# Optimization experiments

Measured on AMD Instinct MI355X. Metric: run time of the kernel, lower is better.

## Reference

```python
import jax, jax.numpy as jnp
import numpy as np

N_HASHES = 4
CHUNK = 144
REDUCTION = 4

# PyTorch bicubic (a=-0.75), align_corners=False, integer scale 2 ->
# fixed fractional offsets t=0.75 (even outputs) and t=0.25 (odd outputs).
_EW = jnp.array([-0.03515625, 0.26171875, 0.87890625, -0.10546875], jnp.float32)
_OW = _EW[::-1]


def _up2_axis(x, axis):
    n = x.shape[axis]
    pad = [(0, 0)] * x.ndim
    pad[axis] = (2, 2)
    xp = jnp.pad(x, pad, mode='edge')  # torch clamps border indices
    sl = lambda s: jax.lax.slice_in_dim(xp, s, s + n, axis=axis)
    even = sum(_EW[k] * sl(k) for k in range(4))
    odd = sum(_OW[k] * sl(k + 1) for k in range(4))
    out = jnp.stack([even, odd], axis=axis + 1)
    shp = list(x.shape)
    shp[axis] = 2 * n
    return out.reshape(shp)


def bicubic_up2(x):
    return _up2_axis(_up2_axis(x, 2), 3)


def conv2d(x, w, b, pad):
    y = jax.lax.conv_general_dilated(x, w, (1, 1), [(pad, pad), (pad, pad)],
                                     dimension_numbers=('NCHW', 'OIHW', 'NCHW'))
    return y + b[None, :, None, None]


def _adj(t):
    # attend to own + two adjacent buckets along chunk axis (axis=2)
    return jnp.concatenate([t, jnp.roll(t, 1, axis=2), jnp.roll(t, -1, axis=2)], axis=3)


def nlsa(x, wm, bm, wa, ba, rot):
    N, Cc, H, W = x.shape
    L = H * W
    xe = conv2d(x, wm, bm, 1).reshape(N, -1, L).transpose(0, 2, 1)  # [N,L,C]
    ye = conv2d(x, wa, ba, 0).reshape(N, -1, L).transpose(0, 2, 1)  # [N,L,C*red]
    C = xe.shape[-1]
    hash_buckets = min(L // CHUNK + (L // CHUNK) % 2, 128)
    # LSH: random rotations -> argmax bucket codes (non-differentiable, detached)
    rotated = jnp.einsum('btf,fhi->bhti', xe, rot)  # [N,h,L,hb//2]
    rotated = jnp.concatenate([rotated, -rotated], axis=-1)  # [N,h,L,hb]
    codes = jnp.argmax(rotated, axis=-1)  # [N,h,L]
    codes = codes + (jnp.arange(N_HASHES) * hash_buckets)[None, :, None]
    codes = jax.lax.stop_gradient(codes.reshape(N, -1))  # [N,h*L]
    indices = jnp.argsort(codes, axis=-1)
    undo = jnp.argsort(indices, axis=-1)
    mod = indices % L
    xs = jnp.take_along_axis(xe, mod[..., None], axis=1)  # [N,h*L,C]
    ys = jnp.take_along_axis(ye, mod[..., None], axis=1)  # [N,h*L,C*red]
    padding = (-L) % CHUNK
    xb = xs.reshape(N, N_HASHES, L, C)
    yb = ys.reshape(N, N_HASHES, L, C * REDUCTION)
    if padding:
        xb = jnp.concatenate([xb, xb[:, :, -padding:, :]], axis=2)
        yb = jnp.concatenate([yb, yb[:, :, -padding:, :]], axis=2)
    nch = xb.shape[2] // CHUNK
    xb = xb.reshape(N, N_HASHES, nch, CHUNK, C)
    yb = yb.reshape(N, N_HASHES, nch, CHUNK, C * REDUCTION)
    xm = xb / jnp.maximum(jnp.linalg.norm(xb, axis=-1, keepdims=True), 5e-5)
    xm = _adj(xm)      # [N,h,k,3*chunk,C]
    ybj = _adj(yb)     # [N,h,k,3*chunk,C*red]
    raw = jnp.einsum('bhkie,bhkje->bhkij', xb, xm)  # [N,h,k,chunk,3*chunk]
    bscore = jax.scipy.special.logsumexp(raw, axis=-1, keepdims=True)
    score = jnp.exp(raw - bscore)
    ret = jnp.einsum('bhkij,bhkje->bhkie', score, ybj)
    ret = ret.reshape(N, N_HASHES, -1, C * REDUCTION)
    bscore = bscore.reshape(N, N_HASHES, -1)
    if padding:
        ret = ret[:, :, :-padding]
        bscore = bscore[:, :, :-padding]
    ret = ret.reshape(N, -1, C * REDUCTION)
    bscore = bscore.reshape(N, -1)
    ret = jnp.take_along_axis(ret, undo[..., None], axis=1)
    bscore = jnp.take_along_axis(bscore, undo, axis=1)
    ret = ret.reshape(N, N_HASHES, L, C * REDUCTION)
    probs = jax.nn.softmax(bscore.reshape(N, N_HASHES, L, 1), axis=1)
    ret = jnp.sum(ret * probs, axis=1)  # [N,L,C*red]
    return ret.transpose(0, 2, 1).reshape(N, -1, H, W) + x


def setup_inputs() -> dict:
    key = jax.random.key(0)
    ks = jax.random.split(key, 8)
    w = lambda k, shape, fan: (jax.random.normal(k, shape, jnp.float32) / np.sqrt(fan)).astype(jnp.float32)
    return {
        'x': jax.random.normal(ks[0], (2, 64, 96, 96), jnp.float32),
        'w1': w(ks[1], (64, 64, 3, 3), 64 * 9), 'b1': jnp.zeros((64,), jnp.float32),
        'w2': w(ks[2], (64, 64, 3, 3), 64 * 9), 'b2': jnp.zeros((64,), jnp.float32),
        'wm': w(ks[3], (16, 64, 3, 3), 64 * 9), 'bm': jnp.zeros((16,), jnp.float32),
        'wa': w(ks[4], (64, 64, 1, 1), 64), 'ba': jnp.zeros((64,), jnp.float32),
        'rot': jax.random.normal(ks[5], (16, N_HASHES, 64), jnp.float32),  # [C, h, hash_buckets//2]
    }


def reference(x, w1, b1, w2, b2, wm, bm, wa, ba, rot):
    x = bicubic_up2(x)
    x = jax.nn.relu(conv2d(x, w1, b1, 1))
    x = jax.nn.relu(conv2d(x, w2, b2, 1))
    return nlsa(x, wm, bm, wa, ba, rot)
```

## Files before the change

kernel.cpp:

```cpp
#include <hip/hip_runtime.h>
#include <math.h>

#define NB 2
#define CIN 64
#define H0 96
#define W0 96
#define HH 192
#define WW 192
#define LL (HH*WW)
#define NHASH 4
#define CHK 144
#define NCHK 256
#define CE 16
#define CV 64
#define NBUCK 128
#define SEGL 576
#define NSEG 64

#define K_ROWB   80
#define V_ROWB   912
#define P_ROWB   72
#define KQ_SZB   34560
#define VT_SZB   58368
#define PST_SZB  10368
#define LKI_SZB  1728
#define QN_SZB   576
#define LDS_T2   (KQ_SZB + VT_SZB + PST_SZB + LKI_SZB + QN_SZB)
#define LDS_T1   (VT_SZB + LKI_SZB)

typedef __attribute__((ext_vector_type(8))) short short8_t;
typedef __attribute__((ext_vector_type(4))) float f32x4;
union FragU { unsigned int u[4]; int4 i; short8_t s; };

__device__ __forceinline__ unsigned int cvtpk_bf16(float a, float b){
  unsigned int r;
  asm("v_cvt_pk_bf16_f32 %0, %1, %2" : "=v"(r) : "v"(a), "v"(b));
  return r;
}
__device__ __forceinline__ float bfl(unsigned int u){ return __uint_as_float(u << 16); }
__device__ __forceinline__ float bfh(unsigned int u){ return __uint_as_float(u & 0xffff0000u); }

__global__ __launch_bounds__(256) void k_upsample(const float* __restrict__ x,
                                                  float* __restrict__ out){
  int idx = blockIdx.x*256 + threadIdx.x;
  if (idx >= NB*CIN*HH*WW) return;
  int ox = idx % WW; int t2 = idx / WW;
  int oy = t2 % HH;  t2 /= HH;
  int i = oy >> 1, a = oy & 1;
  int j = ox >> 1, b = ox & 1;
  const float e0=-0.03515625f, e1=0.26171875f, e2=0.87890625f, e3=-0.10546875f;
  float wy[4], wx[4]; int ty[4], tx[4];
  if (a){ wy[0]=e3; wy[1]=e2; wy[2]=e1; wy[3]=e0; } else { wy[0]=e0; wy[1]=e1; wy[2]=e2; wy[3]=e3; }
  if (b){ wx[0]=e3; wx[1]=e2; wx[2]=e1; wx[3]=e0; } else { wx[0]=e0; wx[1]=e1; wx[2]=e2; wx[3]=e3; }
  int offy = a ? -1 : -2, offx = b ? -1 : -2;
  #pragma unroll
  for (int k=0;k<4;k++){
    int t = i + offy + k; ty[k] = t<0?0:(t>H0-1?H0-1:t);
    int s = j + offx + k; tx[k] = s<0?0:(s>W0-1?W0-1:s);
  }
  const float* xp = x + (size_t)t2*H0*W0;
  float s = 0.f;
  #pragma unroll
  for (int ky=0;ky<4;ky++){
    const float* row = xp + ty[ky]*W0;
    float rs = 0.f;
    rs = fmaf(wx[0], row[tx[0]], rs);
    rs = fmaf(wx[1], row[tx[1]], rs);
    rs = fmaf(wx[2], row[tx[2]], rs);
    rs = fmaf(wx[3], row[tx[3]], rs);
    s = fmaf(wy[ky], rs, s);
  }
  out[idx] = s;
}

__global__ __launch_bounds__(256) void k_prepw(const float* __restrict__ w,
    unsigned short* __restrict__ wsT, int CO){
  int idx = blockIdx.x*256 + threadIdx.x;
  if (idx >= CO*64*9) return;
  int tap = idx % 9; int rem = idx / 9;
  int ci = rem % 64; int co = rem / 64;
  float v = w[(size_t)(co*64 + ci)*9 + tap];
  unsigned int hu = cvtpk_bf16(v, v) & 0xffffu;
  float hf = bfl(hu);
  unsigned int lu = cvtpk_bf16(v - hf, 0.f) & 0xffffu;
  int half = ci >> 5, kg = (ci >> 3) & 3, e = ci & 7;
  size_t base = ((size_t)(tap*2 + half)*2)*CO*32 + ((size_t)co*4 + kg)*8 + e;
  wsT[base]         = (unsigned short)hu;
  wsT[base + (size_t)CO*32] = (unsigned short)lu;
}

template<int CO, bool RELU, bool OUT_NLC>
__global__ __launch_bounds__(256) void k_conv3m(const float* __restrict__ in,
    const unsigned short* __restrict__ wsT, const float* __restrict__ bias,
    float* __restrict__ out){
  __shared__ unsigned short inH[3][66][64];
  __shared__ unsigned short inL[3][66][64];
  const int t = threadIdx.x;
  const int bx = blockIdx.x, y = blockIdx.y, n = blockIdx.z;
  const int x0 = bx*64;
  const int l = t & 63, w = t >> 6;
  const int lq = l & 15, kg = l >> 4;

  for (int e = t; e < 3072; e += 256){
    const int chunk = e & 15;
    const int strip = e >> 4;
    const int ci = strip & 63, row = strip >> 6;
    const int gy = y + row - 1;
    float4 v = make_float4(0.f,0.f,0.f,0.f);
    if (gy >= 0 && gy < HH)
      v = *(const float4*)&in[(((size_t)n*CIN + ci)*HH + gy)*WW + x0 + chunk*4];
    float vv[4] = {v.x, v.y, v.z, v.w};
    #pragma unroll
    for (int j = 0; j < 4; ++j){
      const int col = 1 + chunk*4 + j;
      const int sci = (((ci >> 3) ^ (col & 7)) << 3) | (ci & 7);
      unsigned int hu = cvtpk_bf16(vv[j], vv[j]);
      unsigned int lu = cvtpk_bf16(vv[j] - bfl(hu), 0.f);
      inH[row][col][sci] = (unsigned short)hu;
      inL[row][col][sci] = (unsigned short)lu;
    }
  }
  if (t < 192){
    const int ci = t & 63, row = t >> 6;
    const int gy = y + row - 1;
    const bool okY = (gy >= 0 && gy < HH);
    const float* ip = &in[(((size_t)n*CIN + ci)*HH + (size_t)(okY?gy:0))*WW];
    float vL = (okY && x0 >= 1) ? ip[x0-1] : 0.f;
    float vR = (okY && x0+64 < WW) ? ip[x0+64] : 0.f;
    unsigned int hL = cvtpk_bf16(vL, vL);
    unsigned int lLu = cvtpk_bf16(vL - bfl(hL), 0.f);
    unsigned int hR = cvtpk_bf16(vR, vR);
    unsigned int lRu = cvtpk_bf16(vR - bfl(hR), 0.f);
    const int sci0 = ci;
    const int sci65 = (((ci >> 3) ^ 1) << 3) | (ci & 7);
    inH[row][0][sci0]  = (unsigned short)hL;  inL[row][0][sci0]  = (unsigned short)lLu;
    inH[row][65][sci65] = (unsigned short)hR; inL[row][65][sci65] = (unsigned short)lRu;
  }
  __syncthreads();

  constexpr int NCT = CO/16;
  f32x4 acc[NCT];
  #pragma unroll
  for (int c=0;c<NCT;c++) acc[c] = (f32x4){0.f,0.f,0.f,0.f};
  const unsigned short* wlane = wsT + (size_t)lq*32 + (size_t)kg*8;

  #pragma unroll
  for (int tap=0; tap<9; ++tap){
    const int ky = tap/3, kx = tap - ky*3;
    const int col = w*16 + lq + kx;
    #pragma unroll
    for (int half=0; half<2; ++half){
      const int sci = ((((half<<2) | kg) ^ (col & 7)) << 3);
      FragU Bh, Bl;
      Bh.i = *(const int4*)&inH[ky][col][sci];
      Bl.i = *(const int4*)&inL[ky][col][sci];
      const unsigned short* wth = wlane + (size_t)((tap*2+half)*2)*CO*32;
      #pragma unroll
      for (int ct=0; ct<NCT; ++ct){
        FragU Ah, Al;
        Ah.i = *(const int4*)(wth + ct*512);
        Al.i = *(const int4*)(wth + CO*32 + ct*512);
        acc[ct] = __builtin_amdgcn_mfma_f32_16x16x32_bf16(Ah.s, Bl.s, acc[ct], 0,0,0);
        acc[ct] = __builtin_amdgcn_mfma_f32_16x16x32_bf16(Al.s, Bh.s, acc[ct], 0,0,0);
        acc[ct] = __builtin_amdgcn_mfma_f32_16x16x32_bf16(Ah.s, Bh.s, acc[ct], 0,0,0);
      }
    }
  }

  const int px = x0 + w*16 + lq;
  if constexpr (!OUT_NLC){
    #pragma unroll
    for (int ct=0; ct<NCT; ++ct){
      #pragma unroll
      for (int r=0; r<4; ++r){
        const int co = ct*16 + kg*4 + r;
        float v = acc[ct][r] + bias[co];
        if (RELU) v = fmaxf(v, 0.f);
        out[(((size_t)n*CO + co)*HH + y)*WW + px] = v;
      }
    }
  } else {
    #pragma unroll
    for (int r=0; r<4; ++r){
      const int co = kg*4 + r;
      float v = acc[0][r] + bias[co];
      if (RELU) v = fmaxf(v, 0.f);
      out[((size_t)n*LL + y*WW + px)*CO + co] = v;
    }
  }
}

__global__ __launch_bounds__(256) void k_conv1x1(const float* __restrict__ x2,
    const float* __restrict__ wa, const float* __restrict__ ba,
    unsigned short* __restrict__ yeB){
  __shared__ float xs[64][64];
  __shared__ float wts[64][64];
  const int t = threadIdx.x;
  const int n = blockIdx.y;
  const int l0 = blockIdx.x*64;
  for (int e=t; e<4096; e+=256){
    int ci = e >> 6, l = e & 63;
    xs[ci][l]  = x2[((size_t)n*CIN+ci)*LL + l0 + l];
    wts[ci][l] = wa[(size_t)l*64 + ci];
  }
  __syncthreads();
  const int l = t & 63, cq = t >> 6;
  float acc[16];
  #pragma unroll
  for (int i=0;i<16;i++) acc[i] = ba[cq*16+i];
  for (int ci=0; ci<64; ci++){
    float xv = xs[ci][l];
    #pragma unroll
    for (int i=0;i<16;i++) acc[i] = fmaf(xv, wts[ci][cq*16+i], acc[i]);
  }
  unsigned int wds[8];
  #pragma unroll
  for (int i=0;i<8;i++) wds[i] = cvtpk_bf16(acc[2*i], acc[2*i+1]);
  uint4* op = (uint4*)&yeB[((size_t)n*LL + l0 + l)*64 + cq*16];
  op[0] = make_uint4(wds[0],wds[1],wds[2],wds[3]);
  op[1] = make_uint4(wds[4],wds[5],wds[6],wds[7]);
}

__global__ __launch_bounds__(128) void k_codes(const float* __restrict__ xe,
    const float* __restrict__ rot, unsigned char* __restrict__ codes){
  __shared__ float rs[NHASH][64][16];
  const int t = threadIdx.x;
  for (int e=t; e<4096; e+=128){
    int f = e >> 8; int rem = e & 255;
    int h = rem >> 6; int i = rem & 63;
    rs[h][i][f] = rot[((size_t)f*NHASH + h)*64 + i];
  }
  __syncthreads();
  const int n = blockIdx.y;
  const int l = blockIdx.x*128 + t;
  float q[16];
  const float* xr = &xe[((size_t)n*LL + l)*16];
  #pragma unroll
  for (int f=0;f<16;f++) q[f] = xr[f];
  #pragma unroll
  for (int h=0;h<NHASH;h++){
    float bp = -3.0e38f, bn = -3.0e38f; int ap=0, an=0;
    for (int i=0;i<64;i++){
      float s = 0.f;
      #pragma unroll
      for (int f=0;f<16;f++) s = fmaf(q[f], rs[h][i][f], s);
      if (s > bp){ bp = s; ap = i; }
      if (-s > bn){ bn = -s; an = i; }
    }
    int code = (bp >= bn) ? ap : (64 + an);
    codes[((size_t)n*NHASH + h)*LL + l] = (unsigned char)code;
  }
}

__global__ __launch_bounds__(256) void k_hist(const unsigned char* __restrict__ codes,
    unsigned int* __restrict__ segHist){
  __shared__ unsigned int h[NBUCK];
  const int t = threadIdx.x;
  if (t < NBUCK) h[t] = 0;
  __syncthreads();
  const int n = blockIdx.z, hh = blockIdx.y, s = blockIdx.x;
  const unsigned char* cp = codes + ((size_t)n*NHASH + hh)*LL + (size_t)s*SEGL;
  for (int e=t; e<SEGL; e+=256) atomicAdd(&h[cp[e]], 1u);
  __syncthreads();
  if (t < NBUCK)
    segHist[(((size_t)(n*NHASH+hh))*NSEG + s)*NBUCK + t] = h[t];
}

__global__ __launch_bounds__(128) void k_scan(unsigned int* __restrict__ segHist){
  __shared__ unsigned int tot[NBUCK];
  __shared__ unsigned int base[NBUCK];
  const int b = threadIdx.x;
  const size_t off = (size_t)blockIdx.x * NSEG * NBUCK;
  unsigned int run = 0;
  for (int s=0;s<NSEG;s++){
    unsigned int v = segHist[off + (size_t)s*NBUCK + b];
    segHist[off + (size_t)s*NBUCK + b] = run;
    run += v;
  }
  tot[b] = run;
  __syncthreads();
  if (b==0){ unsigned int r=0; for (int i=0;i<NBUCK;i++){ base[i]=r; r+=tot[i]; } }
  __syncthreads();
  const unsigned int bb = base[b];
  for (int s=0;s<NSEG;s++) segHist[off + (size_t)s*NBUCK + b] += bb;
}

__global__ __launch_bounds__(256) void k_rank(const unsigned char* __restrict__ codes,
    const unsigned int* __restrict__ segHist, int* __restrict__ srtIdx){
  __shared__ unsigned int cw[SEGL/4];
  __shared__ unsigned int sbase[NBUCK];
  const int t = threadIdx.x;
  const int n = blockIdx.z, hh = blockIdx.y, s = blockIdx.x;
  const size_t cb = ((size_t)n*NHASH + hh)*LL + (size_t)s*SEGL;
  const unsigned int* cp32 = (const unsigned int*)(codes + cb);
  for (int e=t; e<SEGL/4; e+=256) cw[e] = cp32[e];
  if (t < NBUCK)
    sbase[t] = segHist[(((size_t)(n*NHASH+hh))*NSEG + s)*NBUCK + t];
  __syncthreads();
  const size_t ob = ((size_t)n*NHASH + hh)*LL;
  for (int e=t; e<SEGL; e+=256){
    unsigned int c = (cw[e>>2] >> ((e&3)*8)) & 0xffu;
    unsigned int mul = c * 0x01010101u;
    int cnt = 0;
    const int nw = e >> 2;
    for (int wi=0; wi<nw; wi++){
      unsigned int v = cw[wi] ^ mul;
      unsigned int t1 = (v & 0x7f7f7f7fu) + 0x7f7f7f7fu;
      unsigned int z = ~(t1 | v) & 0x80808080u;
      cnt += __popc(z);
    }
    unsigned int lastw = cw[nw];
    const int nbp = e & 3;
    for (int bp=0; bp<nbp; bp++)
      if (((lastw >> (bp*8)) & 0xffu) == c) cnt++;
    int pos = (int)sbase[c] + cnt;
    srtIdx[ob + pos] = s*SEGL + e;
  }
}

__global__ __launch_bounds__(256) void k_gatherK(const float* __restrict__ xe,
    const int* __restrict__ srtIdx, unsigned short* __restrict__ Ksrt,
    float* __restrict__ normQ){
  const int idx = blockIdx.x*256 + threadIdx.x;
  if (idx >= NB*NHASH*LL) return;
  const int n = idx / (NHASH*LL);
  const int lk = srtIdx[idx];
  const float4* xr = (const float4*)&xe[((size_t)n*LL + lk)*16];
  float4 v0 = xr[0], v1 = xr[1], v2 = xr[2], v3 = xr[3];
  float f[16] = {v0.x,v0.y,v0.z,v0.w, v1.x,v1.y,v1.z,v1.w,
                 v2.x,v2.y,v2.z,v2.w, v3.x,v3.y,v3.z,v3.w};
  float ss = 0.f;
  #pragma unroll
  for (int i=0;i<16;i++) ss = fmaf(f[i], f[i], ss);
  const float nq = sqrtf(ss);
  normQ[idx] = nq;
  const float inv = 1.f / fmaxf(nq, 5e-5f);
  #pragma unroll
  for (int i=0;i<16;i++) f[i] *= inv;
  unsigned int kh[8], klo[8];
  #pragma unroll
  for (int i=0;i<8;i++) kh[i] = cvtpk_bf16(f[2*i], f[2*i+1]);
  #pragma unroll
  for (int i=0;i<8;i++)
    klo[i] = cvtpk_bf16(f[2*i] - bfl(kh[i]), f[2*i+1] - bfh(kh[i]));
  int4* kr = (int4*)(Ksrt + (size_t)idx*32);
  kr[0] = make_int4((int)kh[0],(int)kh[1],(int)kh[2],(int)kh[3]);
  kr[1] = make_int4((int)kh[4],(int)kh[5],(int)kh[6],(int)kh[7]);
  kr[2] = make_int4((int)klo[0],(int)klo[1],(int)klo[2],(int)klo[3]);
  kr[3] = make_int4((int)klo[4],(int)klo[5],(int)klo[6],(int)klo[7]);
}

__global__ __launch_bounds__(576) void k_attn2t1(const unsigned short* __restrict__ yeB,
    const int* __restrict__ srtIdx, const unsigned short* __restrict__ Ksrt,
    const float* __restrict__ normQ, unsigned short* __restrict__ retS,
    float* __restrict__ bscore){
  extern __shared__ char smem[];
  char* Vt  = smem;
  int* lkI  = (int*)(smem + VT_SZB);
  __shared__ char PstA[9][1024];
  __shared__ char PstB[9][1024];

  const int t = threadIdx.x;
  const int k = blockIdx.x, hh = blockIdx.y, n = blockIdx.z;
  const size_t sb = ((size_t)n*NHASH + hh)*LL;
  const int l = t & 63, w = t >> 6;
  const int lq16 = l & 15, g = l >> 4;

  if (t < 432){
    const int c3 = t / CHK, jl = t - c3*CHK;
    const int kc = (c3==0) ? k : ((c3==1) ? ((k+NCHK-1)&(NCHK-1)) : ((k+1)&(NCHK-1)));
    lkI[t] = srtIdx[sb + (size_t)kc*CHK + jl];
  }
  if (t < 512){
    int c = t >> 3, jp = t & 7;
    *(unsigned int*)(Vt + c*V_ROWB + 864 + jp*4) = 0u;
  }
  __syncthreads();

  #pragma unroll 4
  for (int it=0; it<24; ++it){
    const int e = t + it*576;
    const int jp = e >> 6, c = e & 63;
    const unsigned int a = yeB[((size_t)n*LL + lkI[2*jp  ])*64 + c];
    const unsigned int b = yeB[((size_t)n*LL + lkI[2*jp+1])*64 + c];
    *(unsigned int*)(Vt + c*V_ROWB + jp*4) = a | (b << 16);
  }
  const int qg = w*16 + lq16;
  const int pq = k*CHK + qg;
  const int lqs = lkI[qg];
  FragU b1, b2;
  const unsigned short* qrow = Ksrt + (sb + pq)*32;
  b1.i = *(const int4*)(qrow + (g&1)*8);
  if (g < 2) b2.i = *(const int4*)(qrow + 16 + (g&1)*8);
  else { b2.u[0]=0u; b2.u[1]=0u; b2.u[2]=0u; b2.u[3]=0u; }
  const float nq_ = normQ[sb + pq];
  const float msc = fmaxf(nq_, 5e-5f);
  __syncthreads();

  float sum = 0.f;
  char* const pwA = &PstA[w][0];
  char* const pwB = &PstB[w][0];
  const int pws = lq16*64 + (g&1)*8;
  const int prd = lq16*64 + ((g ^ (lq16&3))<<4);

  auto qksub = [&](int u, char* __restrict__ pw){
    #pragma unroll
    for (int sub=0; sub<2; ++sub){
      const int t27 = 2*u + sub;
      uint2 pwv;
      if (t27 < 27){
        const int c3 = t27 / 9;
        const int kc = (c3==0) ? k : ((c3==1) ? ((k+NCHK-1)&(NCHK-1)) : ((k+1)&(NCHK-1)));
        const int row16 = (t27 - c3*9)*16;
        FragU a; a.i = *(const int4*)(Ksrt + (sb + (size_t)kc*CHK + row16 + lq16)*32 + g*8);
        f32x4 C = {0.f,0.f,0.f,0.f};
        C = __builtin_amdgcn_mfma_f32_16x16x32_bf16(a.s, b2.s, C, 0, 0, 0);
        C = __builtin_amdgcn_mfma_f32_16x16x32_bf16(a.s, b1.s, C, 0, 0, 0);
        const float p0 = __expf(fmaf(msc, C[0], -nq_));
        const float p1 = __expf(fmaf(msc, C[1], -nq_));
        const float p2 = __expf(fmaf(msc, C[2], -nq_));
        const float p3 = __expf(fmaf(msc, C[3], -nq_));
        sum += (p0+p1) + (p2+p3);
        pwv = make_uint2(cvtpk_bf16(p0,p1), cvtpk_bf16(p2,p3));
      } else {
        pwv = make_uint2(0u, 0u);
      }
      const int chunk = (sub*2 + (g>>1)) ^ (lq16 & 3);
      *(uint2*)(pw + pws + (chunk<<4)) = pwv;
    }
  };

  f32x4 O0 = {0.f,0.f,0.f,0.f}, O1 = O0, O2 = O0, O3 = O0;
  qksub(0, pwA);
  #pragma unroll
  for (int uu=0; uu<7; ++uu){
    {
      const int u = 2*uu;
      const char* Vb = Vt + lq16*V_ROWB + u*64 + g*16;
      FragU av0, av1, av2, av3;
      av0.i = *(const int4*)(Vb);
      av1.i = *(const int4*)(Vb + 16*V_ROWB);
      av2.i = *(const int4*)(Vb + 32*V_ROWB);
      av3.i = *(const int4*)(Vb + 48*V_ROWB);
      qksub(u+1, pwB);
      FragU bp; bp.i = *(const int4*)(pwA + prd);
      O0 = __builtin_amdgcn_mfma_f32_16x16x32_bf16(av0.s, bp.s, O0, 0,0,0);
      O1 = __builtin_amdgcn_mfma_f32_16x16x32_bf16(av1.s, bp.s, O1, 0,0,0);
      O2 = __builtin_amdgcn_mfma_f32_16x16x32_bf16(av2.s, bp.s, O2, 0,0,0);
      O3 = __builtin_amdgcn_mfma_f32_16x16x32_bf16(av3.s, bp.s, O3, 0,0,0);
    }
    {
      const int u = 2*uu + 1;
      const char* Vb = Vt + lq16*V_ROWB + u*64 + g*16;
      FragU av0, av1, av2, av3;
      av0.i = *(const int4*)(Vb);
      av1.i = *(const int4*)(Vb + 16*V_ROWB);
      av2.i = *(const int4*)(Vb + 32*V_ROWB);
      av3.i = *(const int4*)(Vb + 48*V_ROWB);
      qksub(u+1, pwA);
      FragU bp; bp.i = *(const int4*)(pwB + prd);
      O0 = __builtin_amdgcn_mfma_f32_16x16x32_bf16(av0.s, bp.s, O0, 0,0,0);
      O1 = __builtin_amdgcn_mfma_f32_16x16x32_bf16(av1.s, bp.s, O1, 0,0,0);
      O2 = __builtin_amdgcn_mfma_f32_16x16x32_bf16(av2.s, bp.s, O2, 0,0,0);
      O3 = __builtin_amdgcn_mfma_f32_16x16x32_bf16(av3.s, bp.s, O3, 0,0,0);
    }
  }
  sum += __shfl_xor(sum, 16);
  sum += __shfl_xor(sum, 32);
  const float linv = 1.f / sum;

  unsigned short* op = &retS[(sb + lqs)*64];
  {
    uint2 s0 = make_uint2(cvtpk_bf16(O0[0]*linv, O0[1]*linv), cvtpk_bf16(O0[2]*linv, O0[3]*linv));
    uint2 s1 = make_uint2(cvtpk_bf16(O1[0]*linv, O1[1]*linv), cvtpk_bf16(O1[2]*linv, O1[3]*linv));
    uint2 s2 = make_uint2(cvtpk_bf16(O2[0]*linv, O2[1]*linv), cvtpk_bf16(O2[2]*linv, O2[3]*linv));
    uint2 s3 = make_uint2(cvtpk_bf16(O3[0]*linv, O3[1]*linv), cvtpk_bf16(O3[2]*linv, O3[3]*linv));
    *(uint2*)(op +  0 + g*4) = s0;
    *(uint2*)(op + 16 + g*4) = s1;
    *(uint2*)(op + 32 + g*4) = s2;
    *(uint2*)(op + 48 + g*4) = s3;
  }
  if (g == 0) bscore[sb + lqs] = nq_ + logf(sum);
}

__global__ __launch_bounds__(576) void k_attn2b(const float* __restrict__ xe,
    const unsigned short* __restrict__ yeB, const int* __restrict__ srtIdx,
    unsigned short* __restrict__ retS, float* __restrict__ bscore){
  extern __shared__ char smem[];
  unsigned short* Kq = (unsigned short*)smem;
  char* Vt  = smem + KQ_SZB;
  char* Pst = Vt + VT_SZB;
  int* lkI  = (int*)(Pst + PST_SZB);
  float* qn = (float*)(Pst + PST_SZB + LKI_SZB);

  const int t = threadIdx.x;
  const int k = blockIdx.x, hh = blockIdx.y, n = blockIdx.z;
  const size_t sb = ((size_t)n*NHASH + hh)*LL;
  const int l = t & 63, w = t >> 6;
  const int lq16 = l & 15, g = l >> 4;

  if (t < 432){
    const int c3 = t / CHK, jl = t - c3*CHK;
    const int kc = (c3==0) ? k : ((c3==1) ? ((k+NCHK-1)&(NCHK-1)) : ((k+1)&(NCHK-1)));
    const int lk = srtIdx[sb + (size_t)kc*CHK + jl];
    lkI[t] = lk;
    const float4* xr = (const float4*)&xe[((size_t)n*LL + lk)*16];
    float4 v0 = xr[0], v1 = xr[1], v2 = xr[2], v3 = xr[3];
    float f[16] = {v0.x,v0.y,v0.z,v0.w, v1.x,v1.y,v1.z,v1.w,
                   v2.x,v2.y,v2.z,v2.w, v3.x,v3.y,v3.z,v3.w};
    float ss = 0.f;
    #pragma unroll
    for (int i=0;i<16;i++) ss = fmaf(f[i], f[i], ss);
    const float nq = sqrtf(ss);
    if (c3 == 0) qn[jl] = nq;
    const float inv = 1.f / fmaxf(nq, 5e-5f);
    #pragma unroll
    for (int i=0;i<16;i++) f[i] *= inv;
    unsigned int kh[8], klo[8];
    #pragma unroll
    for (int i=0;i<8;i++) kh[i] = cvtpk_bf16(f[2*i], f[2*i+1]);
    #pragma unroll
    for (int i=0;i<8;i++)
      klo[i] = cvtpk_bf16(f[2*i] - bfl(kh[i]), f[2*i+1] - bfh(kh[i]));
    int4* kr = (int4*)((char*)Kq + t*K_ROWB);
    kr[0] = make_int4((int)kh[0],(int)kh[1],(int)kh[2],(int)kh[3]);
    kr[1] = make_int4((int)kh[4],(int)kh[5],(int)kh[6],(int)kh[7]);
    kr[2] = make_int4((int)klo[0],(int)klo[1],(int)klo[2],(int)klo[3]);
    kr[3] = make_int4((int)klo[4],(int)klo[5],(int)klo[6],(int)klo[7]);
  }
  if (t < 512){
    int c = t >> 3, jp = t & 7;
    *(unsigned int*)(Vt + c*V_ROWB + 864 + jp*4) = 0u;
  }
  __syncthreads();

  #pragma unroll 4
  for (int it=0; it<24; ++it){
    const int e = t + it*576;
    const int jp = e >> 6, c = e & 63;
    const unsigned int a = yeB[((size_t)n*LL + lkI[2*jp  ])*64 + c];
    const unsigned int b = yeB[((size_t)n*LL + lkI[2*jp+1])*64 + c];
    *(unsigned int*)(Vt + c*V_ROWB + jp*4) = a | (b << 16);
  }
  const int qg = w*16 + lq16;
  const int lqs = lkI[qg];
  FragU b1, b2;
  float nq_;
  {
    const char* qrow = (const char*)Kq + qg*K_ROWB;
    b1.i = *(const int4*)(qrow + (g&1)*16);
    if (g < 2) b2.i = *(const int4*)(qrow + 32 + (g&1)*16);
    else { b2.u[0]=0u; b2.u[1]=0u; b2.u[2]=0u; b2.u[3]=0u; }
    nq_ = qn[qg];
  }
  const float msc = fmaxf(nq_, 5e-5f);
  __syncthreads();

  float sum = 0.f;
  f32x4 O0 = {0.f,0.f,0.f,0.f}, O1 = O0, O2 = O0, O3 = O0;
  char* Pw = Pst + w*(16*P_ROWB);
  for (int u=0; u<14; ++u){
    #pragma unroll
    for (int sub=0; sub<2; ++sub){
      const int t27 = u*2 + sub;
      uint2 pw;
      if (t27 < 27){
        FragU a;
        a.i = *(const int4*)((const char*)Kq + (size_t)(t27*16 + lq16)*K_ROWB + g*16);
        f32x4 C = {0.f,0.f,0.f,0.f};
        C = __builtin_amdgcn_mfma_f32_16x16x32_bf16(a.s, b2.s, C, 0, 0, 0);
        C = __builtin_amdgcn_mfma_f32_16x16x32_bf16(a.s, b1.s, C, 0, 0, 0);
        const float p0 = __expf(fmaf(msc, C[0], -nq_));
        const float p1 = __expf(fmaf(msc, C[1], -nq_));
        const float p2 = __expf(fmaf(msc, C[2], -nq_));
        const float p3 = __expf(fmaf(msc, C[3], -nq_));
        sum += (p0+p1) + (p2+p3);
        pw = make_uint2(cvtpk_bf16(p0,p1), cvtpk_bf16(p2,p3));
      } else {
        pw = make_uint2(0u, 0u);
      }
      *(uint2*)(Pw + lq16*P_ROWB + sub*32 + g*8) = pw;
    }
    asm volatile("s_waitcnt lgkmcnt(0)" ::: "memory");
    __builtin_amdgcn_sched_barrier(0);
    FragU bp; bp.i = *(const int4*)(Pw + lq16*P_ROWB + g*16);
    const char* Vb = Vt + lq16*V_ROWB + u*64 + g*16;
    FragU av;
    av.i = *(const int4*)(Vb);             O0 = __builtin_amdgcn_mfma_f32_16x16x32_bf16(av.s, bp.s, O0, 0,0,0);
    av.i = *(const int4*)(Vb + 16*V_ROWB); O1 = __builtin_amdgcn_mfma_f32_16x16x32_bf16(av.s, bp.s, O1, 0,0,0);
    av.i = *(const int4*)(Vb + 32*V_ROWB); O2 = __builtin_amdgcn_mfma_f32_16x16x32_bf16(av.s, bp.s, O2, 0,0,0);
    av.i = *(const int4*)(Vb + 48*V_ROWB); O3 = __builtin_amdgcn_mfma_f32_16x16x32_bf16(av.s, bp.s, O3, 0,0,0);
  }
  sum += __shfl_xor(sum, 16);
  sum += __shfl_xor(sum, 32);
  const float linv = 1.f / sum;

  unsigned short* op = &retS[(sb + lqs)*64];
  {
    uint2 s0 = make_uint2(cvtpk_bf16(O0[0]*linv, O0[1]*linv), cvtpk_bf16(O0[2]*linv, O0[3]*linv));
    uint2 s1 = make_uint2(cvtpk_bf16(O1[0]*linv, O1[1]*linv), cvtpk_bf16(O1[2]*linv, O1[3]*linv));
    uint2 s2 = make_uint2(cvtpk_bf16(O2[0]*linv, O2[1]*linv), cvtpk_bf16(O2[2]*linv, O2[3]*linv));
    uint2 s3 = make_uint2(cvtpk_bf16(O3[0]*linv, O3[1]*linv), cvtpk_bf16(O3[2]*linv, O3[3]*linv));
    *(uint2*)(op +  0 + g*4) = s0;
    *(uint2*)(op + 16 + g*4) = s1;
    *(uint2*)(op + 32 + g*4) = s2;
    *(uint2*)(op + 48 + g*4) = s3;
  }
  if (g == 0) bscore[sb + lqs] = nq_ + logf(sum);
}

__global__ __launch_bounds__(256) void k_combine(const unsigned short* __restrict__ retS,
    const float* __restrict__ bscore, const float* __restrict__ x2,
    float* __restrict__ out){
  const int idx = blockIdx.x*256 + threadIdx.x;
  if (idx >= NB*LL) return;
  const int l = idx % LL, n = idx / LL;
  float bs[NHASH];
  #pragma unroll
  for (int h=0;h<NHASH;h++)
    bs[h] = bscore[((size_t)n*NHASH + h)*LL + l];
  float m = fmaxf(fmaxf(bs[0],bs[1]), fmaxf(bs[2],bs[3]));
  float wsum = 0.f; float wv[NHASH];
  #pragma unroll
  for (int h=0;h<NHASH;h++){ wv[h] = expf(bs[h]-m); wsum += wv[h]; }
  const float winv = 1.f / wsum;
  float o[64];
  #pragma unroll
  for (int i=0;i<64;i++) o[i]=0.f;
  #pragma unroll
  for (int h=0;h<NHASH;h++){
    const float wh = wv[h]*winv;
    const uint4* rp = (const uint4*)&retS[(((size_t)n*NHASH + h)*LL + l)*64];
    #pragma unroll
    for (int i2=0;i2<8;i2++){
      uint4 v = rp[i2];
      o[i2*8+0] = fmaf(wh, bfl(v.x), o[i2*8+0]);
      o[i2*8+1] = fmaf(wh, bfh(v.x), o[i2*8+1]);
      o[i2*8+2] = fmaf(wh, bfl(v.y), o[i2*8+2]);
      o[i2*8+3] = fmaf(wh, bfh(v.y), o[i2*8+3]);
      o[i2*8+4] = fmaf(wh, bfl(v.z), o[i2*8+4]);
      o[i2*8+5] = fmaf(wh, bfh(v.z), o[i2*8+5]);
      o[i2*8+6] = fmaf(wh, bfl(v.w), o[i2*8+6]);
      o[i2*8+7] = fmaf(wh, bfh(v.w), o[i2*8+7]);
    }
  }
  #pragma unroll
  for (int c=0;c<64;c++){
    size_t oi = ((size_t)n*64 + c)*LL + l;
    out[oi] = o[c] + x2[oi];
  }
}

extern "C" void kernel_launch(void* const* d_in, const int* in_sizes, int n_in,
                              void* d_out, int out_size, void* d_ws, size_t ws_size,
                              hipStream_t stream){
  const float* x   = (const float*)d_in[0];
  const float* w1  = (const float*)d_in[1];
  const float* b1  = (const float*)d_in[2];
  const float* w2  = (const float*)d_in[3];
  const float* b2  = (const float*)d_in[4];
  const float* wm  = (const float*)d_in[5];
  const float* bm  = (const float*)d_in[6];
  const float* wa  = (const float*)d_in[7];
  const float* ba  = (const float*)d_in[8];
  const float* rot = (const float*)d_in[9];
  float* outp = (float*)d_out;
  char* ws = (char*)d_ws;
  const size_t FM   = (size_t)NB*CIN*HH*WW*sizeof(float);
  const size_t YEB  = (size_t)NB*LL*64*2;
  const size_t RETB = (size_t)NB*NHASH*LL*64*2;
  const size_t NHL4 = (size_t)NB*NHASH*LL*4;

  char* p = ws;
  unsigned short* yeB = (unsigned short*)p;  p += YEB;
  char* regA = p;                            p += RETB;
  float* x2  = (float*)p;                    p += FM;
  float* xe  = (float*)p;                    p += (size_t)NB*LL*CE*sizeof(float);
  unsigned char* codes = (unsigned char*)p;  p += (size_t)NB*NHASH*LL;
  unsigned int* segHist = (unsigned int*)p;  p += (size_t)NB*NHASH*NSEG*NBUCK*4;
  int* srtIdx  = (int*)p;                    p += NHL4;
  float* bscore = (float*)p;                 p += NHL4;
  unsigned short* wsT1 = (unsigned short*)p; p += (size_t)9*2*2*64*32*2;
  unsigned short* wsT2 = (unsigned short*)p; p += (size_t)9*2*2*64*32*2;
  unsigned short* wsTm = (unsigned short*)p; p += (size_t)9*2*2*16*32*2;
  const size_t needT2 = (size_t)(p - ws);
  unsigned short* Ksrt = (unsigned short*)p; p += (size_t)NB*NHASH*LL*32*2;
  float* normQ = (float*)p;                  p += NHL4;
  const size_t needT1 = (size_t)(p - ws);

  unsigned short* retS = (unsigned short*)regA;
  float* x0u = (float*)regA;
  float* y1  = (float*)(regA + FM);
  if (ws_size < needT2) return;
  const bool preg = (ws_size >= needT1);

  hipFuncSetAttribute((const void*)k_attn2t1,
                      hipFuncAttributeMaxDynamicSharedMemorySize, LDS_T1);
  hipFuncSetAttribute((const void*)k_attn2b,
                      hipFuncAttributeMaxDynamicSharedMemorySize, LDS_T2);

  k_prepw<<<dim3((64*64*9+255)/256), dim3(256), 0, stream>>>(w1, wsT1, 64);
  k_prepw<<<dim3((64*64*9+255)/256), dim3(256), 0, stream>>>(w2, wsT2, 64);
  k_prepw<<<dim3((16*64*9+255)/256), dim3(256), 0, stream>>>(wm, wsTm, 16);
  k_upsample<<<dim3((NB*CIN*HH*WW+255)/256), dim3(256), 0, stream>>>(x, x0u);
  k_conv3m<64,true,false><<<dim3(3, HH, NB), dim3(256), 0, stream>>>(x0u, wsT1, b1, y1);
  k_conv3m<64,true,false><<<dim3(3, HH, NB), dim3(256), 0, stream>>>(y1, wsT2, b2, x2);
  k_conv3m<16,false,true><<<dim3(3, HH, NB), dim3(256), 0, stream>>>(x2, wsTm, bm, xe);
  k_conv1x1<<<dim3(LL/64, NB), dim3(256), 0, stream>>>(x2, wa, ba, yeB);
  k_codes<<<dim3(LL/128, NB), dim3(128), 0, stream>>>(xe, rot, codes);
  k_hist<<<dim3(NSEG, NHASH, NB), dim3(256), 0, stream>>>(codes, segHist);
  k_scan<<<dim3(NB*NHASH), dim3(128), 0, stream>>>(segHist);
  k_rank<<<dim3(NSEG, NHASH, NB), dim3(256), 0, stream>>>(codes, segHist, srtIdx);
  if (preg){
    k_gatherK<<<dim3((NB*NHASH*LL+255)/256), dim3(256), 0, stream>>>(xe, srtIdx, Ksrt, normQ);
    k_attn2t1<<<dim3(NCHK, NHASH, NB), dim3(576), LDS_T1, stream>>>(
        yeB, srtIdx, Ksrt, normQ, retS, bscore);
  } else {
    k_attn2b<<<dim3(NCHK, NHASH, NB), dim3(576), LDS_T2, stream>>>(
        xe, yeB, srtIdx, retS, bscore);
  }
  k_combine<<<dim3((NB*LL+255)/256), dim3(256), 0, stream>>>(retS, bscore, x2, outp);
}
```

Baseline: 392.2 us.

## Pass softmax probabilities via wave shuffles instead of LDS, swizzle chunk order

The attention kernel no longer stages the bf16 probability tile in per-wave LDS ping-pong buffers. It rebuilds the MFMA B operand directly from the QK accumulator registers with cross-lane shuffles, which removes the LDS round trip and its static shared memory. The loop drops the manual software pipelining, so QK and PV MFMAs are no longer explicitly interleaved. Both attention kernels also remap blockIdx.x to a strided chunk order, likely to change L2 locality or scheduling across chunks.

Result: faster. 366.3 us (-6.6%).

```diff
diff --git a/kernel.cpp b/kernel.cpp
--- a/kernel.cpp
+++ b/kernel.cpp
@@ -350,18 +350,17 @@
   kr[3] = make_int4((int)klo[4],(int)klo[5],(int)klo[6],(int)klo[7]);
 }
 
-__global__ __launch_bounds__(576) void k_attn2t1(const unsigned short* __restrict__ yeB,
+__global__ __launch_bounds__(576) void k_attn4(const unsigned short* __restrict__ yeB,
     const int* __restrict__ srtIdx, const unsigned short* __restrict__ Ksrt,
     const float* __restrict__ normQ, unsigned short* __restrict__ retS,
     float* __restrict__ bscore){
   extern __shared__ char smem[];
   char* Vt  = smem;
   int* lkI  = (int*)(smem + VT_SZB);
-  __shared__ char PstA[9][1024];
-  __shared__ char PstB[9][1024];
 
   const int t = threadIdx.x;
-  const int k = blockIdx.x, hh = blockIdx.y, n = blockIdx.z;
+  const int bx = blockIdx.x, hh = blockIdx.y, n = blockIdx.z;
+  const int k = ((bx & 7) << 5) | (bx >> 3);
   const size_t sb = ((size_t)n*NHASH + hh)*LL;
   const int l = t & 63, w = t >> 6;
   const int lq16 = l & 15, g = l >> 4;
@@ -397,17 +396,18 @@
   const float msc = fmaxf(nq_, 5e-5f);
   __syncthreads();
 
+  const int sl0 = lq16 + ((g & 1) << 5);
+  const int sl1 = sl0 + 16;
+  const bool loTile = (g < 2);
+
   float sum = 0.f;
-  char* const pwA = &PstA[w][0];
-  char* const pwB = &PstB[w][0];
-  const int pws = lq16*64 + (g&1)*8;
-  const int prd = lq16*64 + ((g ^ (lq16&3))<<4);
-
-  auto qksub = [&](int u, char* __restrict__ pw){
+  f32x4 O0 = {0.f,0.f,0.f,0.f}, O1 = O0, O2 = O0, O3 = O0;
+
+  for (int u=0; u<14; ++u){
+    unsigned int pk[2][2];
     #pragma unroll
     for (int sub=0; sub<2; ++sub){
       const int t27 = 2*u + sub;
-      uint2 pwv;
       if (t27 < 27){
         const int c3 = t27 / 9;
         const int kc = (c3==0) ? k : ((c3==1) ? ((k+NCHK-1)&(NCHK-1)) : ((k+1)&(NCHK-1)));
@@ -421,49 +421,32 @@
         const float p2 = __expf(fmaf(msc, C[2], -nq_));
         const float p3 = __expf(fmaf(msc, C[3], -nq_));
         sum += (p0+p1) + (p2+p3);
-        pwv = make_uint2(cvtpk_bf16(p0,p1), cvtpk_bf16(p2,p3));
+        pk[sub][0] = cvtpk_bf16(p0, p1);
+        pk[sub][1] = cvtpk_bf16(p2, p3);
       } else {
-        pwv = make_uint2(0u, 0u);
+        pk[sub][0] = 0u; pk[sub][1] = 0u;
       }
-      const int chunk = (sub*2 + (g>>1)) ^ (lq16 & 3);
-      *(uint2*)(pw + pws + (chunk<<4)) = pwv;
-    }
-  };
-
-  f32x4 O0 = {0.f,0.f,0.f,0.f}, O1 = O0, O2 = O0, O3 = O0;
-  qksub(0, pwA);
-  #pragma unroll
-  for (int uu=0; uu<7; ++uu){
-    {
-      const int u = 2*uu;
-      const char* Vb = Vt + lq16*V_ROWB + u*64 + g*16;
-      FragU av0, av1, av2, av3;
-      av0.i = *(const int4*)(Vb);
-      av1.i = *(const int4*)(Vb + 16*V_ROWB);
-      av2.i = *(const int4*)(Vb + 32*V_ROWB);
-      av3.i = *(const int4*)(Vb + 48*V_ROWB);
-      qksub(u+1, pwB);
-      FragU bp; bp.i = *(const int4*)(pwA + prd);
-      O0 = __builtin_amdgcn_mfma_f32_16x16x32_bf16(av0.s, bp.s, O0, 0,0,0);
-      O1 = __builtin_amdgcn_mfma_f32_16x16x32_bf16(av1.s, bp.s, O1, 0,0,0);
-      O2 = __builtin_amdgcn_mfma_f32_16x16x32_bf16(av2.s, bp.s, O2, 0,0,0);
-      O3 = __builtin_amdgcn_mfma_f32_16x16x32_bf16(av3.s, bp.s, O3, 0,0,0);
-    }
-    {
-      const int u = 2*uu + 1;
-      const char* Vb = Vt + lq16*V_ROWB + u*64 + g*16;
-      FragU av0, av1, av2, av3;
-      av0.i = *(const int4*)(Vb);
-      av1.i = *(const int4*)(Vb + 16*V_ROWB);
-      av2.i = *(const int4*)(Vb + 32*V_ROWB);
-      av3.i = *(const int4*)(Vb + 48*V_ROWB);
-      qksub(u+1, pwA);
-      FragU bp; bp.i = *(const int4*)(pwB + prd);
-      O0 = __builtin_amdgcn_mfma_f32_16x16x32_bf16(av0.s, bp.s, O0, 0,0,0);
-      O1 = __builtin_amdgcn_mfma_f32_16x16x32_bf16(av1.s, bp.s, O1, 0,0,0);
-      O2 = __builtin_amdgcn_mfma_f32_16x16x32_bf16(av2.s, bp.s, O2, 0,0,0);
-      O3 = __builtin_amdgcn_mfma_f32_16x16x32_bf16(av3.s, bp.s, O3, 0,0,0);
-    }
+    }
+    const unsigned int a00 = __shfl(pk[0][0], sl0), a01 = __shfl(pk[0][1], sl0);
+    const unsigned int a10 = __shfl(pk[1][0], sl0), a11 = __shfl(pk[1][1], sl0);
+    const unsigned int b00 = __shfl(pk[0][0], sl1), b01 = __shfl(pk[0][1], sl1);
+    const unsigned int b10 = __shfl(pk[1][0], sl1), b11 = __shfl(pk[1][1], sl1);
+    FragU bp;
+    bp.u[0] = loTile ? a00 : a10;
+    bp.u[1] = loTile ? a01 : a11;
+    bp.u[2] = loTile ? b00 : b10;
+    bp.u[3] = loTile ? b01 : b11;
+
+    const char* Vb = Vt + lq16*V_ROWB + u*64 + g*16;
+    FragU av0, av1, av2, av3;
+    av0.i = *(const int4*)(Vb);
+    av1.i = *(const int4*)(Vb + 16*V_ROWB);
+    av2.i = *(const int4*)(Vb + 32*V_ROWB);
+    av3.i = *(const int4*)(Vb + 48*V_ROWB);
+    O0 = __builtin_amdgcn_mfma_f32_16x16x32_bf16(av0.s, bp.s, O0, 0,0,0);
+    O1 = __builtin_amdgcn_mfma_f32_16x16x32_bf16(av1.s, bp.s, O1, 0,0,0);
+    O2 = __builtin_amdgcn_mfma_f32_16x16x32_bf16(av2.s, bp.s, O2, 0,0,0);
+    O3 = __builtin_amdgcn_mfma_f32_16x16x32_bf16(av3.s, bp.s, O3, 0,0,0);
   }
   sum += __shfl_xor(sum, 16);
   sum += __shfl_xor(sum, 32);
@@ -494,7 +477,8 @@
   float* qn = (float*)(Pst + PST_SZB + LKI_SZB);
 
   const int t = threadIdx.x;
-  const int k = blockIdx.x, hh = blockIdx.y, n = blockIdx.z;
+  const int bx = blockIdx.x, hh = blockIdx.y, n = blockIdx.z;
+  const int k = ((bx & 7) << 5) | (bx >> 3);
   const size_t sb = ((size_t)n*NHASH + hh)*LL;
   const int l = t & 63, w = t >> 6;
   const int lq16 = l & 15, g = l >> 4;
@@ -694,7 +678,7 @@
   if (ws_size < needT2) return;
   const bool preg = (ws_size >= needT1);
 
-  hipFuncSetAttribute((const void*)k_attn2t1,
+  hipFuncSetAttribute((const void*)k_attn4,
                       hipFuncAttributeMaxDynamicSharedMemorySize, LDS_T1);
   hipFuncSetAttribute((const void*)k_attn2b,
                       hipFuncAttributeMaxDynamicSharedMemorySize, LDS_T2);
@@ -713,7 +697,7 @@
   k_rank<<<dim3(NSEG, NHASH, NB), dim3(256), 0, stream>>>(codes, segHist, srtIdx);
   if (preg){
     k_gatherK<<<dim3((NB*NHASH*LL+255)/256), dim3(256), 0, stream>>>(xe, srtIdx, Ksrt, normQ);
-    k_attn2t1<<<dim3(NCHK, NHASH, NB), dim3(576), LDS_T1, stream>>>(
+    k_attn4<<<dim3(NCHK, NHASH, NB), dim3(576), LDS_T1, stream>>>(
         yeB, srtIdx, Ksrt, normQ, retS, bscore);
   } else {
     k_attn2b<<<dim3(NCHK, NHASH, NB), dim3(576), LDS_T2, stream>>>(
```
